# Optimization experiments

Measured on AMD Instinct MI355X. Metric: run time of the kernel, lower is better.

## Reference

```python
import jax, jax.numpy as jnp
import numpy as np

N_SAMPLES = 2 ** 15  # 32768
NYQUIST = 22050.0 / 2.0
MIN_FREQ = 40.0 / NYQUIST
MAX_FREQ = 4000.0 / NYQUIST
FREQ_RANGE = MAX_FREQ - MIN_FREQ


def interp_linear(x, out_size):
    """torch F.interpolate(mode='linear', align_corners=False) along last axis."""
    in_size = x.shape[-1]
    scale = in_size / out_size
    coords = (jnp.arange(out_size, dtype=x.dtype) + 0.5) * scale - 0.5
    coords = jnp.clip(coords, 0.0, in_size - 1)
    lo = jnp.floor(coords).astype(jnp.int32)
    hi = jnp.minimum(lo + 1, in_size - 1)
    w = coords - lo.astype(x.dtype)
    return x[..., lo] * (1.0 - w) + x[..., hi] * w


def translate(pair, shift, scale):
    # angle of complex(pair[:,:,0], pair[:,:,1]) / pi, then affine
    angle = jnp.arctan2(pair[:, :, 1, :], pair[:, :, 0, :]) / np.pi
    return shift + angle * scale


def setup_inputs() -> dict:
    key = jax.random.key(0)
    k1, k2 = jax.random.split(key)
    x = jax.random.normal(k1, (16, 8, 10, 128), dtype=jnp.float32)
    noise = jax.random.normal(k2, (16, 8, N_SAMPLES), dtype=jnp.float32)
    return {"x": x, "noise": noise}


def reference(x, noise):
    # x: (batch, n_osc, 10, time_ctrl); noise: (batch, n_osc, N_SAMPLES)
    basic = x[:, :, 0:2, :]
    amp = jnp.sqrt(jnp.sum(basic * basic, axis=2))            # (b, o, t)
    amp = interp_linear(amp, N_SAMPLES)                       # (b, o, N)

    f0 = translate(basic, MIN_FREQ, FREQ_RANGE)               # control-rate
    mix = interp_linear(translate(x[:, :, 2:4, :], 1.0, 0.5), N_SAMPLES)
    harm_amp = amp * mix
    noise_amp = amp * (1.0 - mix)

    noise_std = translate(x[:, :, 4:6, :], MIN_FREQ, FREQ_RANGE)
    mod_factor = translate(x[:, :, 6:8, :], 0.25, 4.75)
    b = translate(x[:, :, 8:10, :], 0.1, 9.9)

    # band_filtered_noise: narrowband noise as a frequency-jittered sine
    f0_fr = interp_linear(f0, N_SAMPLES)
    std_fr = interp_linear(noise_std, N_SAMPLES)
    bfn = jnp.sin(jnp.cumsum(f0_fr + noise * std_fr, axis=-1))
    noise_sig = noise_amp * bfn

    mod_factor = interp_linear(mod_factor, N_SAMPLES)
    b = interp_linear(b, N_SAMPLES)
    mod = b * jnp.sin(jnp.cumsum(mod_factor, axis=-1))
    sig = harm_amp * jnp.sin(jnp.cumsum(f0_fr, axis=-1) + mod)

    mixed = noise_sig + sig                                   # (b, o, N)
    return jnp.mean(mixed, axis=1, keepdims=True)             # (b, 1, N)
```

## Files before the change

### kernel.cpp

```cpp
#include <hip/hip_runtime.h>
#include <math.h>

#define NS     32768
#define NB     128
#define CELL   8
#define CPB    32
#define PART   (CELL * CPB)
#define NPARTS (NS / PART)
#define TPB    256
#define NBATCH 16
#define GRID   (NBATCH * NPARTS)
#define NBIN   3
#define SJ     ((CELL * (CELL - 1)) / 2)

__device__ __forceinline__ float sinr(float x) {
    return __builtin_amdgcn_sinf(x - rintf(x));
}

__device__ __forceinline__ void seg_params(int i, int& lo, int& hi,
                                           double& w0, double& wst) {
    if (i < 128)            { lo = 0;   hi = 1;   w0 = 0.0; wst = 0.0; }
    else if (i >= NS - 128) { lo = 127; hi = 127; w0 = 0.0; wst = 0.0; }
    else {
        lo = (i - 128) >> 8;  hi = lo + 1;
        int off = (i - 128) & 255;
        w0 = (off + 0.5) * (1.0 / 256.0);
        wst = 1.0 / 256.0;
    }
}

__device__ __forceinline__ double bin_value(const float* xs, int q, int j) {
    const double PI_    = 3.14159265358979323846;
    const double INV2PI = 0.15915494309189533576888376337251;
    const double MINF   = 40.0 / 11025.0;
    const double FRNG   = (4000.0 - 40.0) / 11025.0;
    if (q == 0) {
        double a0 = (double)xs[j], a1 = (double)xs[NB + j];
        return sqrt(a0 * a0 + a1 * a1);
    }
    double ang = atan2((double)xs[(2 * q - 1) * NB + j],
                       (double)xs[(2 * q - 2) * NB + j]) / PI_;
    double sh, sc;
    if      (q == 1) { sh = MINF; sc = FRNG; }
    else if (q == 2) { sh = 1.0;  sc = 0.5;  }
    else if (q == 3) { sh = MINF; sc = FRNG; }
    else if (q == 4) { sh = 0.25; sc = 4.75; }
    else             { sh = 0.1;  sc = 9.9;  }
    double v = sh + ang * sc;
    if (q != 2) v *= INV2PI;
    return v;
}

__device__ __forceinline__ void cell_totals(
        const float4 (&nn)[CELL / 4], double f0L, double dF0, double stL,
        double dSt, double mfL, double dMf, double w0, double wst,
        double& t1, double& t3, double& t2) {
    float s0 = 0.f, s1 = 0.f;
    #pragma unroll
    for (int q4 = 0; q4 < CELL / 4; ++q4) {
        float4 nv = nn[q4];
        float jd = (float)(q4 * 4);
        s0 += nv.x; s1 = fmaf(jd, nv.x, s1);
        s0 += nv.y; s1 = fmaf(jd + 1.f, nv.y, s1);
        s0 += nv.z; s1 = fmaf(jd + 2.f, nv.z, s1);
        s0 += nv.w; s1 = fmaf(jd + 3.f, nv.w, s1);
    }
    double S0 = (double)s0, S1 = (double)s1;
    double sw = (double)CELL * w0 + (double)SJ * wst;
    t3 = (double)CELL * f0L + dF0 * sw;
    t2 = (double)CELL * mfL + dMf * sw;
    t1 = t3 + stL * S0 + dSt * (w0 * S0 + wst * S1);
}

__global__ __launch_bounds__(TPB, 4)
void span_kernel(const float* __restrict__ xg, const float* __restrict__ ng,
                 double* __restrict__ wspan) {
    __shared__ double binsA[8][3][NBIN];

    int bx = blockIdx.x, bb = bx >> 7, p = bx & (NPARTS - 1);
    int tid = threadIdx.x, lane = tid & 63;
    int h = tid >> 5, c = tid & 31;
    int P = p * PART;
    int b0 = (P - 128) >> 8; if (b0 < 0) b0 = 0;
    int s  = (bb << 3) + h;
    int i0 = P + c * CELL;

    const float4* np_ = reinterpret_cast<const float4*>(ng + (size_t)s * NS + i0);
    float4 nv[CELL / 4];
    #pragma unroll
    for (int q4 = 0; q4 < CELL / 4; ++q4) nv[q4] = np_[q4];

    if (tid < 8 * 3 * NBIN) {
        int j = tid % NBIN, r = (tid / NBIN) % 3, h2 = tid / (3 * NBIN);
        int q = (r == 0) ? 1 : (r == 1) ? 3 : 4;
        const float* xs = xg + (size_t)((bb << 3) + h2) * 10 * NB;
        binsA[h2][r][j] = bin_value(xs, q, min(b0 + j, NB - 1));
    }
    __syncthreads();

    int lo, hi; double w0, wst;
    seg_params(i0, lo, hi, w0, wst);
    int jL = lo - b0, jH = hi - b0;
    double f0L = binsA[h][0][jL], dF0 = binsA[h][0][jH] - f0L;
    double stL = binsA[h][1][jL], dSt = binsA[h][1][jH] - stL;
    double mfL = binsA[h][2][jL], dMf = binsA[h][2][jH] - mfL;

    double t1, t3, t2;
    cell_totals(nv, f0L, dF0, stL, dSt, mfL, dMf, w0, wst, t1, t3, t2);

    double v1 = t1, v3 = t3, v2 = t2;
    #pragma unroll
    for (int d = 1; d < 32; d <<= 1) {
        double u1 = __shfl_up(v1, d);
        double u3 = __shfl_up(v3, d);
        double u2 = __shfl_up(v2, d);
        if ((lane & 31) >= d) { v1 += u1; v3 += u3; v2 += u2; }
    }
    if (c == 31) {
        size_t sb = ((size_t)s * NPARTS + p) * 3;
        wspan[sb + 0] = v1; wspan[sb + 1] = v3; wspan[sb + 2] = v2;
    }
}

__global__ __launch_bounds__(TPB, 4)
void fm_kernel(const float* __restrict__ xg, const float* __restrict__ ng,
               const double* __restrict__ wspan, float* __restrict__ out) {
    __shared__ double binsA[8][3][NBIN];
    __shared__ float  binsB[8][6][NBIN];
    __shared__ double wtot[4][8][3];
    __shared__ double prefL[8][3];

    int bx = blockIdx.x, bb = bx >> 7, p = bx & (NPARTS - 1);
    int tid = threadIdx.x, lane = tid & 63, wid = tid >> 6;
    int h = tid & 7, c = tid >> 3;
    int P = p * PART;
    int b0 = (P - 128) >> 8; if (b0 < 0) b0 = 0;
    int s  = (bb << 3) + h;
    int i0 = P + c * CELL;

    const float4* np_ = reinterpret_cast<const float4*>(ng + (size_t)s * NS + i0);
    float4 nv[CELL / 4];
    #pragma unroll
    for (int q4 = 0; q4 < CELL / 4; ++q4) nv[q4] = np_[q4];

    if (tid < 192) {
        int r = tid & 7, g = tid >> 3, k = g % 3, h2 = g / 3;
        const double* sp = wspan + ((size_t)(((bb << 3) + h2) * NPARTS)) * 3 + k;
        double acc = 0.0;
        #pragma unroll
        for (int q = 0; q < NPARTS / 8; ++q) {
            int idx = r + q * 8;
            if (idx < p) acc += sp[idx * 3];
        }
        #pragma unroll
        for (int m = 1; m <= 4; m <<= 1) acc += __shfl_xor(acc, m);
        if (r == 0) prefL[h2][k] = acc;
    }
    if (tid < 8 * 6 * NBIN) {
        int j = tid % NBIN, q = (tid / NBIN) % 6, h2 = tid / (6 * NBIN);
        const float* xs = xg + (size_t)((bb << 3) + h2) * 10 * NB;
        double v = bin_value(xs, q, min(b0 + j, NB - 1));
        binsB[h2][q][j] = (float)v;
        if      (q == 1) binsA[h2][0][j] = v;
        else if (q == 3) binsA[h2][1][j] = v;
        else if (q == 4) binsA[h2][2][j] = v;
    }
    __syncthreads();

    int lo, hi; double w0, wst;
    seg_params(i0, lo, hi, w0, wst);
    int jL = lo - b0, jH = hi - b0;

    double t1, t3, t2;
    {
        double f0L = binsA[h][0][jL], dF0 = binsA[h][0][jH] - f0L;
        double stL = binsA[h][1][jL], dSt = binsA[h][1][jH] - stL;
        double mfL = binsA[h][2][jL], dMf = binsA[h][2][jH] - mfL;
        cell_totals(nv, f0L, dF0, stL, dSt, mfL, dMf, w0, wst, t1, t3, t2);
    }

    double v1 = t1, v3 = t3, v2 = t2;
    #pragma unroll
    for (int d = 8; d < 64; d <<= 1) {
        double u1 = __shfl_up(v1, d);
        double u3 = __shfl_up(v3, d);
        double u2 = __shfl_up(v2, d);
        if (lane >= d) { v1 += u1; v3 += u3; v2 += u2; }
    }
    if (lane >= 56) { wtot[wid][h][0] = v1; wtot[wid][h][1] = v3; wtot[wid][h][2] = v2; }
    __syncthreads();
    double b1 = 0.0, b3 = 0.0, b2 = 0.0;
    #pragma unroll
    for (int k = 0; k < 3; ++k)
        if (wid > k) { b1 += wtot[k][h][0]; b3 += wtot[k][h][1]; b2 += wtot[k][h][2]; }

    double a1 = prefL[h][0] + b1 + (v1 - t1);
    double a3 = prefL[h][1] + b3 + (v3 - t3);
    double a2 = prefL[h][2] + b2 + (v2 - t2);
    float fr1 = (float)(a1 - rint(a1));
    float fr3 = (float)(a3 - rint(a3));
    float fr2 = (float)(a2 - rint(a2));

    float amL = binsB[h][0][jL], dAm = binsB[h][0][jH] - amL;
    float g0L = binsB[h][1][jL], gF0 = binsB[h][1][jH] - g0L;
    float mxL = binsB[h][2][jL], dMx = binsB[h][2][jH] - mxL;
    float gsL = binsB[h][3][jL], gSt = binsB[h][3][jH] - gsL;
    float gmL = binsB[h][4][jL], gMf = binsB[h][4][jH] - gmL;
    float bbL = binsB[h][5][jL], dBb = binsB[h][5][jH] - bbL;
    float w0f = (float)w0, wsf = (float)wst;

    float arr[CELL];
    float d1 = 0.f, d2 = 0.f, d3 = 0.f;
    #pragma unroll
    for (int q4 = 0; q4 < CELL / 4; ++q4) {
        float nf[4] = {nv[q4].x, nv[q4].y, nv[q4].z, nv[q4].w};
        #pragma unroll
        for (int u = 0; u < 4; ++u) {
            int j = q4 * 4 + u;
            float wf  = fmaf((float)j, wsf, w0f);
            float f0v = fmaf(wf, gF0, g0L);
            float stv = fmaf(wf, gSt, gsL);
            float mfv = fmaf(wf, gMf, gmL);
            d3 += f0v;
            d1 += fmaf(nf[u], stv, f0v);
            d2 += mfv;
            float ampv = fmaf(wf, dAm, amL);
            float mixv = fmaf(wf, dMx, mxL);
            float bv   = fmaf(wf, dBb, bbL);
            float s2 = sinr(fr2 + d2);
            float s1 = sinr(fr1 + d1);
            float s3 = sinr(fmaf(bv, s2, fr3 + d3));
            float harm = ampv * mixv;
            arr[j] = fmaf(harm, s3, (ampv - harm) * s1);
        }
    }

    #pragma unroll
    for (int m = 1; m <= 4; m <<= 1) {
        #pragma unroll
        for (int j = 0; j < CELL; ++j) arr[j] += __shfl_xor(arr[j], m);
    }
    if (h == 0) {
        float4* op = reinterpret_cast<float4*>(out + (size_t)bb * NS + i0);
        #pragma unroll
        for (int j4 = 0; j4 < CELL / 4; ++j4)
            op[j4] = make_float4(arr[j4 * 4 + 0] * 0.125f, arr[j4 * 4 + 1] * 0.125f,
                                 arr[j4 * 4 + 2] * 0.125f, arr[j4 * 4 + 3] * 0.125f);
    }
}

extern "C" void kernel_launch(void* const* d_in, const int* in_sizes, int n_in,
                              void* d_out, int out_size, void* d_ws, size_t ws_size,
                              hipStream_t stream) {
    const float* x     = (const float*)d_in[0];
    const float* noise = (const float*)d_in[1];
    float* out = (float*)d_out;
    double* wspan = (double*)d_ws;
    span_kernel<<<GRID, TPB, 0, stream>>>(x, noise, wspan);
    fm_kernel<<<GRID, TPB, 0, stream>>>(x, noise, wspan, out);
}
```

Baseline: 85.03 us.

## Restructure scan into chunk-sum, per-sequence anchor, and float FM kernels

Replaces the two-kernel span/fm scheme with three kernels. A lightweight kernel computes per-128-sample noise moment sums, a per-sequence anchor kernel evaluates all control bins once and scans chunk totals in double to produce wrapped phase offsets per 512-sample part, and the FM kernel then runs its in-block scan in float with 16-sample cells. This removes the redundant per-block atan2 bin evaluation and the serial double prefix loop over prior parts, and it halves the FM grid. The cost is an extra launch and possible precision loss from the float in-block scan.

```diff
diff --git a/kernel.cpp b/kernel.cpp
--- a/kernel.cpp
+++ b/kernel.cpp
@@ -1,31 +1,32 @@
 #include <hip/hip_runtime.h>
 #include <math.h>
 
-#define NS     32768
-#define NB     128
-#define CELL   8
-#define CPB    32
-#define PART   (CELL * CPB)
-#define NPARTS (NS / PART)
-#define TPB    256
-#define NBATCH 16
-#define GRID   (NBATCH * NPARTS)
-#define NBIN   3
-#define SJ     ((CELL * (CELL - 1)) / 2)
+#define NS      32768
+#define NB      128
+#define NSEQ    128
+#define NCHUNK  256
+#define CHUNK   128
+#define CELL    16
+#define PART    512
+#define NPARTS  (NS / PART)
+#define TPB     256
+#define NBATCH  16
+#define NBIN    4
+#define SJ      ((CELL * (CELL - 1)) / 2)
 
 __device__ __forceinline__ float sinr(float x) {
     return __builtin_amdgcn_sinf(x - rintf(x));
 }
 
-__device__ __forceinline__ void seg_params(int i, int& lo, int& hi,
-                                           double& w0, double& wst) {
-    if (i < 128)            { lo = 0;   hi = 1;   w0 = 0.0; wst = 0.0; }
-    else if (i >= NS - 128) { lo = 127; hi = 127; w0 = 0.0; wst = 0.0; }
+__device__ __forceinline__ void seg_params_f(int i, int& lo, int& hi,
+                                             float& w0, float& wst) {
+    if (i < 128)            { lo = 0;   hi = 1;   w0 = 0.f; wst = 0.f; }
+    else if (i >= NS - 128) { lo = 127; hi = 127; w0 = 0.f; wst = 0.f; }
     else {
         lo = (i - 128) >> 8;  hi = lo + 1;
         int off = (i - 128) & 255;
-        w0 = (off + 0.5) * (1.0 / 256.0);
-        wst = 1.0 / 256.0;
+        w0 = (float)(off + 0.5f) * (1.0f / 256.0f);
+        wst = 1.0f / 256.0f;
     }
 }
 
@@ -51,86 +52,116 @@
     return v;
 }
 
-__device__ __forceinline__ void cell_totals(
-        const float4 (&nn)[CELL / 4], double f0L, double dF0, double stL,
-        double dSt, double mfL, double dMf, double w0, double wst,
-        double& t1, double& t3, double& t2) {
-    float s0 = 0.f, s1 = 0.f;
-    #pragma unroll
-    for (int q4 = 0; q4 < CELL / 4; ++q4) {
-        float4 nv = nn[q4];
-        float jd = (float)(q4 * 4);
-        s0 += nv.x; s1 = fmaf(jd, nv.x, s1);
-        s0 += nv.y; s1 = fmaf(jd + 1.f, nv.y, s1);
-        s0 += nv.z; s1 = fmaf(jd + 2.f, nv.z, s1);
-        s0 += nv.w; s1 = fmaf(jd + 3.f, nv.w, s1);
-    }
-    double S0 = (double)s0, S1 = (double)s1;
-    double sw = (double)CELL * w0 + (double)SJ * wst;
-    t3 = (double)CELL * f0L + dF0 * sw;
-    t2 = (double)CELL * mfL + dMf * sw;
-    t1 = t3 + stL * S0 + dSt * (w0 * S0 + wst * S1);
-}
-
-__global__ __launch_bounds__(TPB, 4)
-void span_kernel(const float* __restrict__ xg, const float* __restrict__ ng,
-                 double* __restrict__ wspan) {
-    __shared__ double binsA[8][3][NBIN];
-
-    int bx = blockIdx.x, bb = bx >> 7, p = bx & (NPARTS - 1);
-    int tid = threadIdx.x, lane = tid & 63;
-    int h = tid >> 5, c = tid & 31;
-    int P = p * PART;
-    int b0 = (P - 128) >> 8; if (b0 < 0) b0 = 0;
-    int s  = (bb << 3) + h;
-    int i0 = P + c * CELL;
-
-    const float4* np_ = reinterpret_cast<const float4*>(ng + (size_t)s * NS + i0);
-    float4 nv[CELL / 4];
-    #pragma unroll
-    for (int q4 = 0; q4 < CELL / 4; ++q4) nv[q4] = np_[q4];
-
-    if (tid < 8 * 3 * NBIN) {
-        int j = tid % NBIN, r = (tid / NBIN) % 3, h2 = tid / (3 * NBIN);
-        int q = (r == 0) ? 1 : (r == 1) ? 3 : 4;
-        const float* xs = xg + (size_t)((bb << 3) + h2) * 10 * NB;
-        binsA[h2][r][j] = bin_value(xs, q, min(b0 + j, NB - 1));
-    }
-    __syncthreads();
-
-    int lo, hi; double w0, wst;
-    seg_params(i0, lo, hi, w0, wst);
-    int jL = lo - b0, jH = hi - b0;
-    double f0L = binsA[h][0][jL], dF0 = binsA[h][0][jH] - f0L;
-    double stL = binsA[h][1][jL], dSt = binsA[h][1][jH] - stL;
-    double mfL = binsA[h][2][jL], dMf = binsA[h][2][jH] - mfL;
-
+__global__ __launch_bounds__(TPB)
+void sum_kernel(const float* __restrict__ ng, float* __restrict__ chunkS) {
+    int bid = blockIdx.x;
+    int seq = bid >> 5, blk = bid & 31;
+    int t = threadIdx.x;
+    int ck = t >> 5, l = t & 31;
+    int base = blk * 1024 + ck * CHUNK + l * 4;
+    const float4 nv = *reinterpret_cast<const float4*>(
+        ng + (size_t)seq * NS + base);
+    float j0 = (float)(l * 4);
+    float s0 = nv.x + nv.y + nv.z + nv.w;
+    float s1 = fmaf(j0, nv.x, fmaf(j0 + 1.f, nv.y,
+               fmaf(j0 + 2.f, nv.z, (j0 + 3.f) * nv.w)));
+    #pragma unroll
+    for (int m = 1; m <= 16; m <<= 1) {
+        s0 += __shfl_xor(s0, m);
+        s1 += __shfl_xor(s1, m);
+    }
+    if (l == 0) {
+        int chunk = blk * 8 + ck;
+        float2* o = reinterpret_cast<float2*>(
+            chunkS + ((size_t)seq * NCHUNK + chunk) * 2);
+        *o = make_float2(s0, s1);
+    }
+}
+
+__global__ __launch_bounds__(TPB)
+void anchor_kernel(const float* __restrict__ xg, const float* __restrict__ chunkS,
+                   float* __restrict__ binsG, float* __restrict__ frG) {
+    __shared__ double bf[3][NB];
+    __shared__ double wsum[4][3];
+
+    int seq = blockIdx.x;
+    int t = threadIdx.x;
+    const float* xs = xg + (size_t)seq * 10 * NB;
+
+    for (int idx = t; idx < 6 * NB; idx += TPB) {
+        int q = idx >> 7, j = idx & (NB - 1);
+        double v = bin_value(xs, q, j);
+        binsG[((size_t)seq * 6 + q) * NB + j] = (float)v;
+        if      (q == 1) bf[0][j] = v;
+        else if (q == 3) bf[1][j] = v;
+        else if (q == 4) bf[2][j] = v;
+    }
+    __syncthreads();
+
+    int c = t;
+    float2 sv = *reinterpret_cast<const float2*>(
+        chunkS + ((size_t)seq * NCHUNK + c) * 2);
+    double S0 = (double)sv.x, S1 = (double)sv.y;
     double t1, t3, t2;
-    cell_totals(nv, f0L, dF0, stL, dSt, mfL, dMf, w0, wst, t1, t3, t2);
-
+    if (c == 0) {
+        t3 = 128.0 * bf[0][0];
+        t2 = 128.0 * bf[2][0];
+        t1 = t3 + bf[1][0] * S0;
+    } else if (c == NCHUNK - 1) {
+        t3 = 128.0 * bf[0][NB - 1];
+        t2 = 128.0 * bf[2][NB - 1];
+        t1 = t3 + bf[1][NB - 1] * S0;
+    } else {
+        int k = (c - 1) >> 1, hf = (c - 1) & 1;
+        double sw  = 64.0 * (double)hf + 32.0;
+        double f0L = bf[0][k], dF0 = bf[0][k + 1] - f0L;
+        double stL = bf[1][k], dSt = bf[1][k + 1] - stL;
+        double mfL = bf[2][k], dMf = bf[2][k + 1] - mfL;
+        t3 = 128.0 * f0L + dF0 * sw;
+        t2 = 128.0 * mfL + dMf * sw;
+        t1 = t3 + stL * S0
+                + dSt * ((128.0 * (double)hf + 0.5) * S0 + S1) * (1.0 / 256.0);
+    }
+
+    int lane = t & 63, wid = t >> 6;
     double v1 = t1, v3 = t3, v2 = t2;
     #pragma unroll
-    for (int d = 1; d < 32; d <<= 1) {
+    for (int d = 1; d < 64; d <<= 1) {
         double u1 = __shfl_up(v1, d);
         double u3 = __shfl_up(v3, d);
         double u2 = __shfl_up(v2, d);
-        if ((lane & 31) >= d) { v1 += u1; v3 += u3; v2 += u2; }
-    }
-    if (c == 31) {
-        size_t sb = ((size_t)s * NPARTS + p) * 3;
-        wspan[sb + 0] = v1; wspan[sb + 1] = v3; wspan[sb + 2] = v2;
+        if (lane >= d) { v1 += u1; v3 += u3; v2 += u2; }
+    }
+    if (lane == 63) { wsum[wid][0] = v1; wsum[wid][1] = v3; wsum[wid][2] = v2; }
+    __syncthreads();
+    double b1 = 0.0, b3 = 0.0, b2 = 0.0;
+    #pragma unroll
+    for (int k = 0; k < 3; ++k)
+        if (wid > k) { b1 += wsum[k][0]; b3 += wsum[k][1]; b2 += wsum[k][2]; }
+    v1 += b1; v3 += b3; v2 += b2;
+
+    if ((c & 3) == 3 && c < 4 * (NPARTS - 1)) {
+        int p = (c >> 2) + 1;
+        float* o = frG + ((size_t)seq * NPARTS + p) * 3;
+        o[0] = (float)(v1 - rint(v1));
+        o[1] = (float)(v3 - rint(v3));
+        o[2] = (float)(v2 - rint(v2));
+    }
+    if (c == 0) {
+        float* o = frG + (size_t)seq * NPARTS * 3;
+        o[0] = 0.f; o[1] = 0.f; o[2] = 0.f;
     }
 }
 
 __global__ __launch_bounds__(TPB, 4)
-void fm_kernel(const float* __restrict__ xg, const float* __restrict__ ng,
-               const double* __restrict__ wspan, float* __restrict__ out) {
-    __shared__ double binsA[8][3][NBIN];
-    __shared__ float  binsB[8][6][NBIN];
-    __shared__ double wtot[4][8][3];
-    __shared__ double prefL[8][3];
-
-    int bx = blockIdx.x, bb = bx >> 7, p = bx & (NPARTS - 1);
+void fm_kernel(const float* __restrict__ ng, const float* __restrict__ binsG,
+               const float* __restrict__ frG, float* __restrict__ out) {
+    __shared__ float binsB[8][6][NBIN];
+    __shared__ float frL[8][3];
+    __shared__ float wtot[4][8][3];
+
+    int bx = blockIdx.x;
+    int bb = bx >> 6, p = bx & (NPARTS - 1);
     int tid = threadIdx.x, lane = tid & 63, wid = tid >> 6;
     int h = tid & 7, c = tid >> 3;
     int P = p * PART;
@@ -144,62 +175,19 @@
     for (int q4 = 0; q4 < CELL / 4; ++q4) nv[q4] = np_[q4];
 
     if (tid < 192) {
-        int r = tid & 7, g = tid >> 3, k = g % 3, h2 = g / 3;
-        const double* sp = wspan + ((size_t)(((bb << 3) + h2) * NPARTS)) * 3 + k;
-        double acc = 0.0;
-        #pragma unroll
-        for (int q = 0; q < NPARTS / 8; ++q) {
-            int idx = r + q * 8;
-            if (idx < p) acc += sp[idx * 3];
-        }
-        #pragma unroll
-        for (int m = 1; m <= 4; m <<= 1) acc += __shfl_xor(acc, m);
-        if (r == 0) prefL[h2][k] = acc;
-    }
-    if (tid < 8 * 6 * NBIN) {
-        int j = tid % NBIN, q = (tid / NBIN) % 6, h2 = tid / (6 * NBIN);
-        const float* xs = xg + (size_t)((bb << 3) + h2) * 10 * NB;
-        double v = bin_value(xs, q, min(b0 + j, NB - 1));
-        binsB[h2][q][j] = (float)v;
-        if      (q == 1) binsA[h2][0][j] = v;
-        else if (q == 3) binsA[h2][1][j] = v;
-        else if (q == 4) binsA[h2][2][j] = v;
-    }
-    __syncthreads();
-
-    int lo, hi; double w0, wst;
-    seg_params(i0, lo, hi, w0, wst);
+        int j = tid & 3, q = (tid >> 2) % 6, h2 = tid / 24;
+        binsB[h2][q][j] =
+            binsG[((size_t)((bb << 3) + h2) * 6 + q) * NB + min(b0 + j, NB - 1)];
+    }
+    if (tid < 24) {
+        int k = tid % 3, h2 = tid / 3;
+        frL[h2][k] = frG[((size_t)((bb << 3) + h2) * NPARTS + p) * 3 + k];
+    }
+    __syncthreads();
+
+    int lo, hi; float w0, wst;
+    seg_params_f(i0, lo, hi, w0, wst);
     int jL = lo - b0, jH = hi - b0;
-
-    double t1, t3, t2;
-    {
-        double f0L = binsA[h][0][jL], dF0 = binsA[h][0][jH] - f0L;
-        double stL = binsA[h][1][jL], dSt = binsA[h][1][jH] - stL;
-        double mfL = binsA[h][2][jL], dMf = binsA[h][2][jH] - mfL;
-        cell_totals(nv, f0L, dF0, stL, dSt, mfL, dMf, w0, wst, t1, t3, t2);
-    }
-
-    double v1 = t1, v3 = t3, v2 = t2;
-    #pragma unroll
-    for (int d = 8; d < 64; d <<= 1) {
-        double u1 = __shfl_up(v1, d);
-        double u3 = __shfl_up(v3, d);
-        double u2 = __shfl_up(v2, d);
-        if (lane >= d) { v1 += u1; v3 += u3; v2 += u2; }
-    }
-    if (lane >= 56) { wtot[wid][h][0] = v1; wtot[wid][h][1] = v3; wtot[wid][h][2] = v2; }
-    __syncthreads();
-    double b1 = 0.0, b3 = 0.0, b2 = 0.0;
-    #pragma unroll
-    for (int k = 0; k < 3; ++k)
-        if (wid > k) { b1 += wtot[k][h][0]; b3 += wtot[k][h][1]; b2 += wtot[k][h][2]; }
-
-    double a1 = prefL[h][0] + b1 + (v1 - t1);
-    double a3 = prefL[h][1] + b3 + (v3 - t3);
-    double a2 = prefL[h][2] + b2 + (v2 - t2);
-    float fr1 = (float)(a1 - rint(a1));
-    float fr3 = (float)(a3 - rint(a3));
-    float fr2 = (float)(a2 - rint(a2));
 
     float amL = binsB[h][0][jL], dAm = binsB[h][0][jH] - amL;
     float g0L = binsB[h][1][jL], gF0 = binsB[h][1][jH] - g0L;
@@ -207,7 +195,39 @@
     float gsL = binsB[h][3][jL], gSt = binsB[h][3][jH] - gsL;
     float gmL = binsB[h][4][jL], gMf = binsB[h][4][jH] - gmL;
     float bbL = binsB[h][5][jL], dBb = binsB[h][5][jH] - bbL;
-    float w0f = (float)w0, wsf = (float)wst;
+
+    float s0 = 0.f, s1 = 0.f;
+    #pragma unroll
+    for (int q4 = 0; q4 < CELL / 4; ++q4) {
+        float jd = (float)(q4 * 4);
+        s0 += nv[q4].x; s1 = fmaf(jd,       nv[q4].x, s1);
+        s0 += nv[q4].y; s1 = fmaf(jd + 1.f, nv[q4].y, s1);
+        s0 += nv[q4].z; s1 = fmaf(jd + 2.f, nv[q4].z, s1);
+        s0 += nv[q4].w; s1 = fmaf(jd + 3.f, nv[q4].w, s1);
+    }
+    float sw = (float)CELL * w0 + (float)SJ * wst;
+    float t3 = (float)CELL * g0L + gF0 * sw;
+    float t2 = (float)CELL * gmL + gMf * sw;
+    float t1 = t3 + gsL * s0 + gSt * fmaf(w0, s0, wst * s1);
+
+    float v1 = t1, v3 = t3, v2 = t2;
+    #pragma unroll
+    for (int d = 8; d < 64; d <<= 1) {
+        float u1 = __shfl_up(v1, d);
+        float u3 = __shfl_up(v3, d);
+        float u2 = __shfl_up(v2, d);
+        if (lane >= d) { v1 += u1; v3 += u3; v2 += u2; }
+    }
+    if (lane >= 56) { wtot[wid][h][0] = v1; wtot[wid][h][1] = v3; wtot[wid][h][2] = v2; }
+    __syncthreads();
+    float b1 = 0.f, b3 = 0.f, b2 = 0.f;
+    #pragma unroll
+    for (int k = 0; k < 3; ++k)
+        if (wid > k) { b1 += wtot[k][h][0]; b3 += wtot[k][h][1]; b2 += wtot[k][h][2]; }
+
+    float fr1 = frL[h][0] + b1 + (v1 - t1); fr1 -= rintf(fr1);
+    float fr3 = frL[h][1] + b3 + (v3 - t3); fr3 -= rintf(fr3);
+    float fr2 = frL[h][2] + b2 + (v2 - t2); fr2 -= rintf(fr2);
 
     float arr[CELL];
     float d1 = 0.f, d2 = 0.f, d3 = 0.f;
@@ -217,7 +237,7 @@
         #pragma unroll
         for (int u = 0; u < 4; ++u) {
             int j = q4 * 4 + u;
-            float wf  = fmaf((float)j, wsf, w0f);
+            float wf  = fmaf((float)j, wst, w0);
             float f0v = fmaf(wf, gF0, g0L);
             float stv = fmaf(wf, gSt, gsL);
             float mfv = fmaf(wf, gMf, gmL);
@@ -228,10 +248,10 @@
             float mixv = fmaf(wf, dMx, mxL);
             float bv   = fmaf(wf, dBb, bbL);
             float s2 = sinr(fr2 + d2);
-            float s1 = sinr(fr1 + d1);
-            float s3 = sinr(fmaf(bv, s2, fr3 + d3));
+            float sA = sinr(fr1 + d1);
+            float sB = sinr(fmaf(bv, s2, fr3 + d3));
             float harm = ampv * mixv;
-            arr[j] = fmaf(harm, s3, (ampv - harm) * s1);
+            arr[j] = fmaf(harm, sB, (ampv - harm) * sA);
         }
     }
 
@@ -255,7 +275,10 @@
     const float* x     = (const float*)d_in[0];
     const float* noise = (const float*)d_in[1];
     float* out = (float*)d_out;
-    double* wspan = (double*)d_ws;
-    span_kernel<<<GRID, TPB, 0, stream>>>(x, noise, wspan);
-    fm_kernel<<<GRID, TPB, 0, stream>>>(x, noise, wspan, out);
-}
+    float* chunkS = (float*)d_ws;
+    float* binsG  = (float*)((char*)d_ws + 262144);
+    float* frG    = (float*)((char*)d_ws + 262144 + 393216);
+    sum_kernel<<<NSEQ * 32, TPB, 0, stream>>>(noise, chunkS);
+    anchor_kernel<<<NSEQ, TPB, 0, stream>>>(x, chunkS, binsG, frG);
+    fm_kernel<<<NBATCH * NPARTS, TPB, 0, stream>>>(noise, binsG, frG, out);
+}
```

Result: faster. 81.57 us (-4.1%).
